# Kernel tuning notes

Hardware: AMD Instinct MI355X
Metric: run time of the kernel (lower is better)

## Reference

```python
import jax, jax.numpy as jnp
import numpy as np

BLOCK, HALO, HEADS, DH = 8, 4, 4, 32
EPS = 1e-5


def _convT(x, w, p):
    # torch ConvTranspose2d(stride=1, padding=p) == conv with flipped/transposed kernel, padding k-1-p
    k = w.shape[-1]
    w2 = jnp.flip(w, axis=(-2, -1)).transpose(1, 0, 2, 3)  # (Cin,Cout,k,k) -> (Cout,Cin,k,k)
    pad = k - 1 - p
    return jax.lax.conv_general_dilated(x, w2, (1, 1), ((pad, pad), (pad, pad)),
                                        dimension_numbers=('NCHW', 'OIHW', 'NCHW'))


def _bn(x, g, b, m, v):
    s = g * jax.lax.rsqrt(v + EPS)
    return x * s[None, :, None, None] + (b - m * s)[None, :, None, None]


def _rel_to_abs(x):
    # x: [b, l, 2r-1] -> [b, l, r]
    b, l, m = x.shape
    r = (m + 1) // 2
    x = jnp.concatenate([x, jnp.zeros((b, l, 1), x.dtype)], axis=2)
    flat = jnp.concatenate([x.reshape(b, l * (m + 1)), jnp.zeros((b, m - l), x.dtype)], axis=1)
    return flat.reshape(b, l + 1, m)[:, :l, -r:]


def _rel_logits_1d(q, rel_k):
    # q: [b, x, y, d]; rel_k: [2r-1, d] -> [b, x, r, y, r]
    b, x, y, d = q.shape
    r = (rel_k.shape[0] + 1) // 2
    logits = jnp.einsum('bxyd,rd->bxyr', q, rel_k)
    logits = _rel_to_abs(logits.reshape(b * x, y, -1)).reshape(b, x, y, r)
    return jnp.broadcast_to(logits[:, :, None, :, :], (b, x, r, y, r))


def _rel_pos_emb(q, rel_h, rel_w):
    # q: [bb, block*block, dh] (already scaled, per halonet-pytorch)
    bb, n, d = q.shape
    qg = q.reshape(bb, BLOCK, BLOCK, d)
    lw = _rel_logits_1d(qg, rel_w).transpose(0, 1, 3, 2, 4).reshape(bb, n, -1)  # b (x y) (i j)
    lh = _rel_logits_1d(qg.transpose(0, 2, 1, 3), rel_h).transpose(0, 3, 1, 4, 2).reshape(bb, n, -1)  # b (y x) (j i)
    return lw + lh


def _halo_attn(x, to_q, to_kv, to_out_w, to_out_b, rel_h, rel_w):
    B, C, H, W = x.shape
    b, h = BLOCK, HALO
    nh, nw = H // b, W // b
    nblk = nh * nw
    wsz = b + 2 * h
    inner = to_q.shape[1]
    scale = DH ** -0.5
    # queries: non-overlapping blocks -> [B*nblk, b*b, C]
    q_inp = x.reshape(B, C, nh, b, nw, b).transpose(0, 2, 4, 3, 5, 1).reshape(B * nblk, b * b, C)
    # keys/values: overlapping halo windows (F.unfold) -> [B*nblk, wsz*wsz, C]
    pat = jax.lax.conv_general_dilated_patches(x, (wsz, wsz), (b, b), ((h, h), (h, h)))  # [B, C*wsz*wsz, nh, nw]
    kv_inp = pat.reshape(B, C, wsz * wsz, nblk).transpose(0, 3, 2, 1).reshape(B * nblk, wsz * wsz, C)
    q = q_inp @ to_q
    k, v = jnp.split(kv_inp @ to_kv, 2, axis=-1)
    def heads(t):
        return t.reshape(t.shape[0], t.shape[1], HEADS, DH).transpose(0, 2, 1, 3).reshape(-1, t.shape[1], DH)
    q, k, v = heads(q) * scale, heads(k), heads(v)
    sim = jnp.einsum('bid,bjd->bij', q, k) + _rel_pos_emb(q, rel_h, rel_w)  # [B*nblk*HEADS, b*b, wsz*wsz]
    # mask out halo positions that fall into zero padding
    ones = jnp.ones((1, 1, H, W), x.dtype)
    mpat = jax.lax.conv_general_dilated_patches(ones, (wsz, wsz), (b, b), ((h, h), (h, h)))
    mask = mpat.reshape(wsz * wsz, nblk).T > 0  # [nblk, wsz*wsz]
    neg = -jnp.finfo(sim.dtype).max
    sim = jnp.where(mask[None, :, None, None, :],
                    sim.reshape(B, nblk, HEADS, b * b, wsz * wsz), neg)
    attn = jax.nn.softmax(sim, axis=-1).reshape(-1, b * b, wsz * wsz)
    out = jnp.einsum('bij,bjd->bid', attn, v)
    out = out.reshape(B * nblk, HEADS, b * b, DH).transpose(0, 2, 1, 3).reshape(B * nblk, b * b, inner)
    out = out @ to_out_w + to_out_b
    return out.reshape(B, nh, nw, b, b, C).transpose(0, 5, 1, 3, 2, 4).reshape(B, C, H, W)


def setup_inputs() -> dict:
    key = jax.random.key(0)
    ks = jax.random.split(key, 13)
    B, C, H, W = 2, 128, 192, 192
    inner = HEADS * DH
    rel = 2 * (BLOCK + 2 * HALO) - 1  # 31
    n = lambda k, s, sc: jax.random.normal(k, s, jnp.float32) * sc
    return {
        'x': jax.random.normal(ks[0], (B, C, H, W), jnp.float32),
        'conv1_w': n(ks[1], (C, C, 1, 1), 0.1),
        'bn1_g': jnp.ones((C,), jnp.float32), 'bn1_b': jnp.zeros((C,), jnp.float32),
        'bn1_m': n(ks[2], (C,), 0.1),
        'bn1_v': jax.random.uniform(ks[3], (C,), jnp.float32, 0.5, 1.5),
        'to_q': n(ks[4], (C, inner), 0.05), 'to_kv': n(ks[5], (C, 2 * inner), 0.05),
        'to_out_w': n(ks[6], (inner, C), 0.05), 'to_out_b': n(ks[7], (C,), 0.01),
        'rel_h': n(ks[8], (rel, DH), DH ** -0.5), 'rel_w': n(ks[9], (rel, DH), DH ** -0.5),
        'conv3_w': n(ks[10], (C, C, 3, 3), 0.05),
        'bn3_g': jnp.ones((C,), jnp.float32), 'bn3_b': jnp.zeros((C,), jnp.float32),
        'bn3_m': n(ks[11], (C,), 0.1),
        'bn3_v': jax.random.uniform(ks[12], (C,), jnp.float32, 0.5, 1.5),
    }


def reference(x, conv1_w, bn1_g, bn1_b, bn1_m, bn1_v, to_q, to_kv, to_out_w, to_out_b,
              rel_h, rel_w, conv3_w, bn3_g, bn3_b, bn3_m, bn3_v):
    # Bottleneck (stride=1, no downsample): conv1x1T -> BN -> ReLU -> HaloAttention -> ReLU
    #   -> conv3x3T -> BN -> +identity -> ReLU
    out = jax.nn.relu(_bn(_convT(x, conv1_w, 0), bn1_g, bn1_b, bn1_m, bn1_v))
    out = jax.nn.relu(_halo_attn(out, to_q, to_kv, to_out_w, to_out_b, rel_h, rel_w))
    out = _bn(_convT(out, conv3_w, 1), bn3_g, bn3_b, bn3_m, bn3_v)
    return jax.nn.relu(out + x)
```

## Files before the change

### kernel.cpp

```cpp
#include <hip/hip_runtime.h>
#include <hip/hip_bf16.h>

using bf16 = __hip_bfloat16;
typedef unsigned short u16;
typedef unsigned int   u32;
typedef __attribute__((ext_vector_type(8))) short short8;
typedef __attribute__((ext_vector_type(4))) float f32x4;

#define B_N 2
#define CCH 128
#define HH 192
#define WW 192
#define HWS (HH*WW)
#define NPIX (B_N*HWS)
#define NBLKS 576
#define EPSV 1e-5f
#define LDW 136

__device__ __forceinline__ float b2f(bf16 v){ return __bfloat162float(v); }
__device__ __forceinline__ bf16  f2b(float v){ return __float2bfloat16(v); }
__device__ __forceinline__ u16  bits(bf16 v){ return *(u16*)&v; }
__device__ __forceinline__ u32 pck(float a, float b){
    bf16 x = f2b(a), y = f2b(b);
    return (u32)*(u16*)&x | ((u32)*(u16*)&y << 16);
}

__global__ __launch_bounds__(256) void transpose_in(const float* __restrict__ x,
                                                    bf16* __restrict__ xT)
{
    __shared__ float tile[128][17];
    const int t   = threadIdx.x;
    const int hw0 = blockIdx.x * 16;
    const int n   = hw0 / HWS;
    const int hwl = hw0 - n*HWS;
    const int px = t & 15, cb = t >> 4;
    #pragma unroll
    for (int r = 0; r < 8; ++r){
        int ci = r*16 + cb;
        tile[ci][px] = x[(size_t)(n*CCH + ci)*HWS + hwl + px];
    }
    __syncthreads();
    const int pix = t >> 4, cig = t & 15;
    uint4 pk;
    pk.x = pck(tile[cig*8+0][pix], tile[cig*8+1][pix]);
    pk.y = pck(tile[cig*8+2][pix], tile[cig*8+3][pix]);
    pk.z = pck(tile[cig*8+4][pix], tile[cig*8+5][pix]);
    pk.w = pck(tile[cig*8+6][pix], tile[cig*8+7][pix]);
    *(uint4*)&xT[(size_t)(hw0 + pix)*CCH + cig*8] = pk;
}

__global__ __launch_bounds__(256) void prep_w(
    const float* __restrict__ w1, const float* __restrict__ to_q,
    const float* __restrict__ to_kv, const float* __restrict__ to_ow,
    const float* __restrict__ w3, const float* __restrict__ relh,
    const float* __restrict__ relw, bf16* __restrict__ wb)
{
    int i = blockIdx.x*256 + threadIdx.x;
    if (i >= 231360) return;
    float v;
    if (i < 16384){       int co=(i>>7)&127, ci=i&127;      v = w1[ci*128+co]; }
    else if (i < 32768){  int r=i-16384; int co=r>>7, ci=r&127; v = to_q[ci*128+co]*0.17677669529663687f; }
    else if (i < 49152){  int r=i-32768; int co=r>>7, ci=r&127; v = to_kv[ci*256+co]; }
    else if (i < 65536){  int r=i-49152; int co=r>>7, ci=r&127; v = to_kv[ci*256+128+co]; }
    else if (i < 81920){  int r=i-65536; int co=r>>7, ci=r&127; v = to_ow[ci*128+co]; }
    else if (i < 229376){ int r=i-81920; int tap=r>>14, co=(r>>7)&127, ci=r&127; int a=tap/3, b=tap-a*3;
                          v = w3[((size_t)(ci*128+co)*3+a)*3+b]; }
    else if (i < 230368){ v = relh[i-229376]; }
    else                { v = relw[i-230368]; }
    wb[i] = f2b(v);
}

template<bool DO_BN, bool DO_BIAS, bool DO_RELU, bool TRANS_Y2>
__global__ __launch_bounds__(256) void gemm_mfma(
    const bf16* __restrict__ inp, const bf16* __restrict__ Wp,
    bf16* __restrict__ outp, bf16* __restrict__ outp2, int cstride, int choff,
    const float* __restrict__ bn_g, const float* __restrict__ bn_b,
    const float* __restrict__ bn_m, const float* __restrict__ bn_v,
    const float* __restrict__ bias)
{
    Wp    += (size_t)blockIdx.y * 16384;
    choff += blockIdx.y * 128;
    __shared__ u16 sW[128*LDW];
    __shared__ u16 sX[64*LDW];
    const int tid  = threadIdx.x;
    const int pix0 = blockIdx.x * 64;
    const int lane = tid & 63;
    const int ln = lane & 15, g = lane >> 4;
    const int cow = (tid >> 6) * 32;

    #pragma unroll
    for (int r = 0; r < 8; ++r){
        int e = tid + r*256; int row = e>>4, grp = e&15;
        *(uint4*)&sW[row*LDW + grp*8] = *(const uint4*)&Wp[row*128 + grp*8];
    }
    #pragma unroll
    for (int r = 0; r < 4; ++r){
        int e = tid + r*256; int row = e>>4, grp = e&15;
        *(uint4*)&sX[row*LDW + grp*8] = *(const uint4*)&inp[(size_t)(pix0+row)*CCH + grp*8];
    }
    __syncthreads();

    f32x4 acc[4][2];
    #pragma unroll
    for (int mi=0;mi<4;mi++)
        #pragma unroll
        for (int ni=0;ni<2;ni++) acc[mi][ni] = (f32x4){0.f,0.f,0.f,0.f};

    #pragma unroll
    for (int kk = 0; kk < 4; ++kk){
        short8 fa[4], fb[2];
        #pragma unroll
        for (int mi=0;mi<4;mi++)
            fa[mi] = *(const short8*)&sX[(mi*16+ln)*LDW + kk*32 + g*8];
        #pragma unroll
        for (int ni=0;ni<2;ni++)
            fb[ni] = *(const short8*)&sW[(cow+ni*16+ln)*LDW + kk*32 + g*8];
        #pragma unroll
        for (int mi=0;mi<4;mi++)
            #pragma unroll
            for (int ni=0;ni<2;ni++)
                acc[mi][ni] = __builtin_amdgcn_mfma_f32_16x16x32_bf16(fa[mi], fb[ni], acc[mi][ni], 0, 0, 0);
    }

    if (TRANS_Y2 && blockIdx.y == 2){
        __syncthreads();
        u16* tile = sX;
        #pragma unroll
        for (int mi=0;mi<4;mi++)
            #pragma unroll
            for (int ni=0;ni<2;ni++){
                int co   = cow + ni*16 + ln;
                int pixl = mi*16 + g*4;
                *(u32*)&tile[co*68 + pixl]     = pck(acc[mi][ni][0], acc[mi][ni][1]);
                *(u32*)&tile[co*68 + pixl + 2] = pck(acc[mi][ni][2], acc[mi][ni][3]);
            }
        __syncthreads();
        const int co2 = tid >> 1, hf = tid & 1;
        const int n2 = pix0 / HWS, hwb2 = pix0 - n2*HWS;
        u16* gdst = (u16*)outp2 + (size_t)(n2*CCH + co2)*HWS + hwb2 + hf*32;
        const u16* src = &tile[co2*68 + hf*32];
        #pragma unroll
        for (int k=0;k<8;k++)
            *(uint2*)&gdst[k*4] = *(const uint2*)&src[k*4];
        return;
    }

    float sc[2], bb[2];
    #pragma unroll
    for (int ni=0;ni<2;ni++){
        int co = cow + ni*16 + ln;
        sc[ni] = 1.f; bb[ni] = 0.f;
        if (DO_BN){ float sg = bn_g[co]*rsqrtf(bn_v[co]+EPSV); sc[ni]=sg; bb[ni]=bn_b[co]-bn_m[co]*sg; }
        if (DO_BIAS) bb[ni] += bias[co];
    }
    #pragma unroll
    for (int mi=0;mi<4;mi++)
        #pragma unroll
        for (int ni=0;ni<2;ni++)
            #pragma unroll
            for (int j=0;j<4;j++){
                int pix = pix0 + mi*16 + g*4 + j;
                int co  = cow + ni*16 + ln;
                float v = acc[mi][ni][j]*sc[ni] + bb[ni];
                if (DO_RELU) v = fmaxf(v, 0.f);
                outp[(size_t)pix*cstride + choff + co] = f2b(v);
            }
}

__global__ __launch_bounds__(256) void conv3_mfma(
    const bf16* __restrict__ inp, const bf16* __restrict__ W3p,
    const float* __restrict__ xin, float* __restrict__ outp,
    const float* __restrict__ g3, const float* __restrict__ b3,
    const float* __restrict__ m3, const float* __restrict__ v3)
{
    __shared__ u16 sW[128*LDW];
    __shared__ u16 sX[64*LDW];
    const int tid = threadIdx.x;
    const int P0  = blockIdx.x * 64;
    const int n   = P0 / HWS;
    const int hwb = P0 - n*HWS;
    const int h = hwb / WW, wb = hwb - h*WW;
    const int lane = tid & 63, ln = lane & 15, g = lane >> 4;
    const int cow = (tid >> 6) * 32;

    f32x4 acc[2][4];
    #pragma unroll
    for (int mi=0;mi<2;mi++)
        #pragma unroll
        for (int ni=0;ni<4;ni++) acc[mi][ni] = (f32x4){0.f,0.f,0.f,0.f};

    for (int tap = 0; tap < 9; ++tap){
        const int a = tap/3, b = tap - a*3;
        const int hs = h + 1 - a;
        if (hs < 0 || hs >= HH) continue;
        const int ws0 = wb + 1 - b;
        __syncthreads();
        #pragma unroll
        for (int r = 0; r < 8; ++r){
            int e = tid + r*256; int row = e>>4, grp = e&15;
            *(uint4*)&sW[row*LDW + grp*8] = *(const uint4*)&W3p[tap*16384 + row*128 + grp*8];
        }
        #pragma unroll
        for (int r = 0; r < 4; ++r){
            int e = tid + r*256; int row = e>>4, grp = e&15;
            int wsrc = ws0 + row;
            uint4 val = {0u,0u,0u,0u};
            if (wsrc >= 0 && wsrc < WW)
                val = *(const uint4*)&inp[(size_t)(n*HWS + hs*WW + wsrc)*CCH + grp*8];
            *(uint4*)&sX[row*LDW + grp*8] = val;
        }
        __syncthreads();
        #pragma unroll
        for (int kk = 0; kk < 4; ++kk){
            short8 fa[2], fb[4];
            #pragma unroll
            for (int mi=0;mi<2;mi++)
                fa[mi] = *(const short8*)&sW[(cow+mi*16+ln)*LDW + kk*32 + g*8];
            #pragma unroll
            for (int ni=0;ni<4;ni++)
                fb[ni] = *(const short8*)&sX[(ni*16+ln)*LDW + kk*32 + g*8];
            #pragma unroll
            for (int mi=0;mi<2;mi++)
                #pragma unroll
                for (int ni=0;ni<4;ni++)
                    acc[mi][ni] = __builtin_amdgcn_mfma_f32_16x16x32_bf16(fa[mi], fb[ni], acc[mi][ni], 0, 0, 0);
        }
    }

    #pragma unroll
    for (int mi=0;mi<2;mi++)
        #pragma unroll
        for (int j=0;j<4;j++){
            int co = cow + mi*16 + g*4 + j;
            float sg = g3[co]*rsqrtf(v3[co]+EPSV);
            float bc = b3[co] - m3[co]*sg;
            #pragma unroll
            for (int ni=0;ni<4;ni++){
                int pixl = hwb + ni*16 + ln;
                size_t idx = (size_t)(n*CCH + co)*HWS + pixl;
                float v = acc[mi][ni][j]*sg + bc + xin[idx];
                outp[idx] = fmaxf(v, 0.f);
            }
        }
}

__global__ __launch_bounds__(512) void attn_kernel(
    const u16* __restrict__ QK, const u16* __restrict__ vT,
    const u16* __restrict__ relb, bf16* __restrict__ outp)
{
    __shared__ __align__(16) char smem[60160];
    u16*   sQb  = (u16*)(smem);
    u16*   sK   = (u16*)(smem + 5120);
    u16*   sRH  = (u16*)(smem + 25600);
    u16*   sRW  = (u16*)(smem + 28160);
    u16*   sP   = (u16*)(smem);
    u16*   sVT  = (u16*)(smem + 33792);
    float* tT   = (float*)(smem + 50688);
    float* wredM= (float*)(smem + 59136);
    float* wredS= (float*)(smem + 59648);

    const int tid  = threadIdx.x;
    const int bid0 = blockIdx.x;
    const int bid  = (bid0 & 7) * 576 + (bid0 >> 3);
    const int head = bid & 3;
    const int t    = bid >> 2;
    const int n    = t / NBLKS;
    const int blk  = t - n*NBLKS;
    const int bi = blk / 24, bj = blk - bi*24;
    const int row0 = bi*8 - 4, col0 = bj*8 - 4;
    const int ch0 = head*32;
    const int wv = tid >> 6, lane = tid & 63, ln = lane & 15, g = lane >> 4;
    const int nt = wv & 3, mh = wv >> 2;

    for (int e = tid; e < 1024; e += 512){
        int r = e >> 5, d = e & 31;
        sRH[r*40 + d] = (r < 31) ? relb[r*32 + d]       : (u16)0;
        sRW[r*40 + d] = (r < 31) ? relb[992 + r*32 + d] : (u16)0;
    }
    {
        int qq = tid >> 3, db = tid & 7;
        size_t P = (size_t)n*HWS + (bi*8 + (qq>>3))*WW + bj*8 + (qq&7);
        *(uint2*)&sQb[qq*40 + db*4] = *(const uint2*)&QK[P*256 + ch0 + db*4];
    }
    #pragma unroll
    for (int r = 0; r < 4; ++r){
        int e = tid + r*512;
        int wp = e >> 3, db = e & 7;
        int rr = row0 + (wp>>4), cc2 = col0 + (wp&15);
        uint2 kk2 = {0u,0u};
        if (rr>=0 && rr<HH && cc2>=0 && cc2<WW){
            size_t P = (size_t)n*HWS + rr*WW + cc2;
            kk2 = *(const uint2*)&QK[P*256 + 128 + ch0 + db*4];
        }
        *(uint2*)&sK[wp*40 + db*4] = kk2;
    }
    #pragma unroll
    for (int r = 0; r < 4; ++r){
        int e = tid + r*512;
        int d   = e >> 6;
        int rem = e & 63;
        int iw  = rem >> 2;
        int jc  = (rem & 3) * 4;
        int rr  = row0 + iw, cc0 = col0 + jc;
        uint2 vv = {0u,0u};
        if (rr >= 0 && rr < HH && cc0 >= 0 && cc0 < 189)
            vv = *(const uint2*)&vT[(size_t)(n*CCH + ch0 + d)*HWS + rr*WW + cc0];
        *(uint2*)&sVT[d*264 + iw*16 + jc] = vv;
    }
    __syncthreads();

    const short8 qfrag = *(const short8*)&sQb[(nt*16+ln)*40 + g*8];
    f32x4 accs[8];
    #pragma unroll
    for (int i=0;i<8;i++){
        short8 fk = *(const short8*)&sK[((mh*8+i)*16+ln)*40 + g*8];
        accs[i] = __builtin_amdgcn_mfma_f32_16x16x32_bf16(fk, qfrag, (f32x4){0.f,0.f,0.f,0.f}, 0, 0, 0);
    }

    {
        const u16* sRX = mh ? sRW : sRH;
        #pragma unroll
        for (int ntr=0; ntr<2; ++ntr){
            short8 fr = *(const short8*)&sRX[(ntr*16+ln)*40 + g*8];
            f32x4 L = __builtin_amdgcn_mfma_f32_16x16x32_bf16(qfrag, fr, (f32x4){0.f,0.f,0.f,0.f}, 0, 0, 0);
            #pragma unroll
            for (int r2=0;r2<4;r2++){
                int q  = nt*16 + g*4 + r2;
                int rr = ntr*16 + ln;
                int bq = mh ? (q&7) : (q>>3);
                int iw = rr - 15 + bq;
                if (iw >= 0 && iw < 16) tT[mh*1056 + iw*66 + q] = L[r2];
            }
        }
    }
    __syncthreads();

    const int qc = nt*16 + ln;
    float tw[4];
    bool cok[4];
    #pragma unroll
    for (int r2=0;r2<4;r2++){
        tw[r2] = tT[1056 + (g*4+r2)*66 + qc];
        int cc2 = col0 + g*4 + r2;
        cok[r2] = (cc2 >= 0 && cc2 < WW);
    }
    float mx = -3.4e38f;
    #pragma unroll
    for (int i=0;i<8;i++){
        int mt = mh*8 + i;
        int rr = row0 + mt;
        bool rok = (rr >= 0 && rr < HH);
        float th = tT[mt*66 + qc];
        #pragma unroll
        for (int r2=0;r2<4;r2++){
            float s = (rok && cok[r2]) ? (accs[i][r2] + th + tw[r2]) : -3.0e38f;
            accs[i][r2] = s;
            mx = fmaxf(mx, s);
        }
    }
    mx = fmaxf(mx, __shfl_xor(mx, 16));
    mx = fmaxf(mx, __shfl_xor(mx, 32));
    if (g == 0) wredM[mh*64 + qc] = mx;
    __syncthreads();
    mx = fmaxf(wredM[qc], wredM[64 + qc]);

    float sm = 0.f;
    #pragma unroll
    for (int i=0;i<8;i++){
        int mt = mh*8 + i;
        float p0 = __expf(accs[i][0]-mx);
        float p1 = __expf(accs[i][1]-mx);
        float p2 = __expf(accs[i][2]-mx);
        float p3 = __expf(accs[i][3]-mx);
        sm += (p0+p1)+(p2+p3);
        u32* dst = (u32*)&sP[qc*264 + mt*16 + g*4];
        dst[0] = pck(p0,p1);
        dst[1] = pck(p2,p3);
    }
    sm += __shfl_xor(sm, 16);
    sm += __shfl_xor(sm, 32);
    if (g == 0) wredS[mh*64 + qc] = sm;
    __syncthreads();

    const int dt = wv & 1, qt = wv >> 1;
    f32x4 acco = (f32x4){0.f,0.f,0.f,0.f};
    #pragma unroll
    for (int ks=0; ks<8; ++ks){
        short8 fa = *(const short8*)&sVT[(dt*16+ln)*264 + ks*32 + g*8];
        short8 fb = *(const short8*)&sP [(qt*16+ln)*264 + ks*32 + g*8];
        acco = __builtin_amdgcn_mfma_f32_16x16x32_bf16(fa, fb, acco, 0, 0, 0);
    }
    {
        const int q = qt*16 + ln;
        const float inv = 1.f / (wredS[q] + wredS[64 + q]);
        size_t P = (size_t)n*HWS + (bi*8 + (q>>3))*WW + bj*8 + (q&7);
        uint2 ov;
        ov.x = pck(acco[0]*inv, acco[1]*inv);
        ov.y = pck(acco[2]*inv, acco[3]*inv);
        *(uint2*)&outp[P*CCH + ch0 + dt*16 + g*4] = ov;
    }
}

extern "C" void kernel_launch(void* const* d_in, const int* in_sizes, int n_in,
                              void* d_out, int out_size, void* d_ws, size_t ws_size,
                              hipStream_t stream)
{
    (void)in_sizes; (void)n_in; (void)out_size; (void)ws_size;
    const float* x      = (const float*)d_in[0];
    const float* w1     = (const float*)d_in[1];
    const float* bn1_g  = (const float*)d_in[2];
    const float* bn1_b  = (const float*)d_in[3];
    const float* bn1_m  = (const float*)d_in[4];
    const float* bn1_v  = (const float*)d_in[5];
    const float* to_q   = (const float*)d_in[6];
    const float* to_kv  = (const float*)d_in[7];
    const float* to_ow  = (const float*)d_in[8];
    const float* to_ob  = (const float*)d_in[9];
    const float* rel_h  = (const float*)d_in[10];
    const float* rel_w  = (const float*)d_in[11];
    const float* w3     = (const float*)d_in[12];
    const float* bn3_g  = (const float*)d_in[13];
    const float* bn3_b  = (const float*)d_in[14];
    const float* bn3_m  = (const float*)d_in[15];
    const float* bn3_v  = (const float*)d_in[16];

    char* ws   = (char*)d_ws;
    bf16* out1 = (bf16*)(ws + 0);
    bf16* qk   = (bf16*)(ws + 18874368);
    bf16* xT   = (bf16*)(ws + 56623104);
    bf16* vT   = (bf16*)(ws + 75497472);
    bf16* wb   = (bf16*)(ws + 94371840);
    bf16* W3p  = wb + 81920;
    u16*  relb = (u16*)(wb + 229376);
    bf16* attnout = (bf16*)d_out;
    bf16* out2    = out1;

    transpose_in<<<4608, 256, 0, stream>>>(x, xT);
    prep_w<<<904, 256, 0, stream>>>(w1, to_q, to_kv, to_ow, w3, rel_h, rel_w, wb);

    gemm_mfma<true,false,true,false><<<dim3(1152,1), 256, 0, stream>>>(
        xT, wb, out1, nullptr, 128, 0, bn1_g, bn1_b, bn1_m, bn1_v, nullptr);
    gemm_mfma<false,false,false,true><<<dim3(1152,3), 256, 0, stream>>>(
        out1, wb + 16384, qk, vT, 256, 0, nullptr,nullptr,nullptr,nullptr,nullptr);

    attn_kernel<<<4608, 512, 0, stream>>>((const u16*)qk, (const u16*)vT,
                                          relb, attnout);

    gemm_mfma<false,true,true,false><<<dim3(1152,1), 256, 0, stream>>>(
        attnout, wb + 65536, out2, nullptr, 128, 0, nullptr,nullptr,nullptr,nullptr, to_ob);

    conv3_mfma<<<1152, 256, 0, stream>>>(out2, W3p, x, (float*)d_out,
                                         bn3_g, bn3_b, bn3_m, bn3_v);
}
```

Measured before the change: 185.3 us.

## Fuse input transpose into conv1 GEMM and shrink attention shared memory

Removes the separate transpose_in kernel: conv1_mfma now reads the fp32 NCHW input directly, transposes and converts it to bf16 in shared memory, and runs the 1x1 conv GEMM with BN+ReLU in the same kernel. The aim is to cut one launch and the round trip of the xT intermediate through global memory. The attention kernel loads Q and the relative-position tables straight from global memory instead of staging them in LDS, and pads the rel tables in prep_w to 32 rows. It also splits the P·V product into two halves that reuse a half-size sP buffer, which adds syncs but reduces LDS use to raise occupancy.

```diff
diff --git a/kernel.cpp b/kernel.cpp
--- a/kernel.cpp
+++ b/kernel.cpp
@@ -12,41 +12,15 @@
 #define HH 192
 #define WW 192
 #define HWS (HH*WW)
-#define NPIX (B_N*HWS)
 #define NBLKS 576
 #define EPSV 1e-5f
 #define LDW 136
 
 __device__ __forceinline__ float b2f(bf16 v){ return __bfloat162float(v); }
 __device__ __forceinline__ bf16  f2b(float v){ return __float2bfloat16(v); }
-__device__ __forceinline__ u16  bits(bf16 v){ return *(u16*)&v; }
 __device__ __forceinline__ u32 pck(float a, float b){
     bf16 x = f2b(a), y = f2b(b);
     return (u32)*(u16*)&x | ((u32)*(u16*)&y << 16);
-}
-
-__global__ __launch_bounds__(256) void transpose_in(const float* __restrict__ x,
-                                                    bf16* __restrict__ xT)
-{
-    __shared__ float tile[128][17];
-    const int t   = threadIdx.x;
-    const int hw0 = blockIdx.x * 16;
-    const int n   = hw0 / HWS;
-    const int hwl = hw0 - n*HWS;
-    const int px = t & 15, cb = t >> 4;
-    #pragma unroll
-    for (int r = 0; r < 8; ++r){
-        int ci = r*16 + cb;
-        tile[ci][px] = x[(size_t)(n*CCH + ci)*HWS + hwl + px];
-    }
-    __syncthreads();
-    const int pix = t >> 4, cig = t & 15;
-    uint4 pk;
-    pk.x = pck(tile[cig*8+0][pix], tile[cig*8+1][pix]);
-    pk.y = pck(tile[cig*8+2][pix], tile[cig*8+3][pix]);
-    pk.z = pck(tile[cig*8+4][pix], tile[cig*8+5][pix]);
-    pk.w = pck(tile[cig*8+6][pix], tile[cig*8+7][pix]);
-    *(uint4*)&xT[(size_t)(hw0 + pix)*CCH + cig*8] = pk;
 }
 
 __global__ __launch_bounds__(256) void prep_w(
@@ -56,7 +30,6 @@
     const float* __restrict__ relw, bf16* __restrict__ wb)
 {
     int i = blockIdx.x*256 + threadIdx.x;
-    if (i >= 231360) return;
     float v;
     if (i < 16384){       int co=(i>>7)&127, ci=i&127;      v = w1[ci*128+co]; }
     else if (i < 32768){  int r=i-16384; int co=r>>7, ci=r&127; v = to_q[ci*128+co]*0.17677669529663687f; }
@@ -65,17 +38,99 @@
     else if (i < 81920){  int r=i-65536; int co=r>>7, ci=r&127; v = to_ow[ci*128+co]; }
     else if (i < 229376){ int r=i-81920; int tap=r>>14, co=(r>>7)&127, ci=r&127; int a=tap/3, b=tap-a*3;
                           v = w3[((size_t)(ci*128+co)*3+a)*3+b]; }
-    else if (i < 230368){ v = relh[i-229376]; }
-    else                { v = relw[i-230368]; }
+    else if (i < 230400){ int j=i-229376; v = (j < 992) ? relh[j] : 0.f; }
+    else                { int j=i-230400; v = (j < 992) ? relw[j] : 0.f; }
     wb[i] = f2b(v);
 }
 
-template<bool DO_BN, bool DO_BIAS, bool DO_RELU, bool TRANS_Y2>
+__global__ __launch_bounds__(256) void conv1_mfma(
+    const float* __restrict__ x, const bf16* __restrict__ Wp,
+    bf16* __restrict__ outp,
+    const float* __restrict__ bn_g, const float* __restrict__ bn_b,
+    const float* __restrict__ bn_m, const float* __restrict__ bn_v)
+{
+    __shared__ float tF[128*68];
+    __shared__ u16   sX[64*LDW];
+    u16* sW = (u16*)tF;
+    const int tid  = threadIdx.x;
+    const int pix0 = blockIdx.x * 64;
+    const int n    = pix0 / HWS;
+    const int hwb  = pix0 - n*HWS;
+    const int lane = tid & 63;
+    const int ln = lane & 15, g = lane >> 4;
+    const int cow = (tid >> 6) * 32;
+
+    #pragma unroll
+    for (int r = 0; r < 32; ++r){
+        int e = tid + r*256;
+        int ci = e >> 6, px = e & 63;
+        tF[ci*68 + px] = x[(size_t)(n*CCH + ci)*HWS + hwb + px];
+    }
+    __syncthreads();
+    {
+        const int pix = tid & 63, cq = tid >> 6;
+        u32 pkt[16];
+        #pragma unroll
+        for (int c = 0; c < 16; ++c){
+            int ci = cq*32 + c*2;
+            pkt[c] = pck(tF[ci*68 + pix], tF[(ci+1)*68 + pix]);
+        }
+        u32* dst = (u32*)&sX[pix*LDW + cq*32];
+        #pragma unroll
+        for (int c = 0; c < 16; ++c) dst[c] = pkt[c];
+    }
+    __syncthreads();
+    #pragma unroll
+    for (int r = 0; r < 8; ++r){
+        int e = tid + r*256; int row = e>>4, grp = e&15;
+        *(uint4*)&sW[row*LDW + grp*8] = *(const uint4*)&Wp[row*128 + grp*8];
+    }
+    __syncthreads();
+
+    f32x4 acc[4][2];
+    #pragma unroll
+    for (int mi=0;mi<4;mi++)
+        #pragma unroll
+        for (int ni=0;ni<2;ni++) acc[mi][ni] = (f32x4){0.f,0.f,0.f,0.f};
+    #pragma unroll
+    for (int kk = 0; kk < 4; ++kk){
+        short8 fa[4], fb[2];
+        #pragma unroll
+        for (int mi=0;mi<4;mi++)
+            fa[mi] = *(const short8*)&sX[(mi*16+ln)*LDW + kk*32 + g*8];
+        #pragma unroll
+        for (int ni=0;ni<2;ni++)
+            fb[ni] = *(const short8*)&sW[(cow+ni*16+ln)*LDW + kk*32 + g*8];
+        #pragma unroll
+        for (int mi=0;mi<4;mi++)
+            #pragma unroll
+            for (int ni=0;ni<2;ni++)
+                acc[mi][ni] = __builtin_amdgcn_mfma_f32_16x16x32_bf16(fa[mi], fb[ni], acc[mi][ni], 0, 0, 0);
+    }
+    float sc[2], bb[2];
+    #pragma unroll
+    for (int ni=0;ni<2;ni++){
+        int co = cow + ni*16 + ln;
+        float sg = bn_g[co]*rsqrtf(bn_v[co]+EPSV);
+        sc[ni] = sg; bb[ni] = bn_b[co] - bn_m[co]*sg;
+    }
+    #pragma unroll
+    for (int mi=0;mi<4;mi++)
+        #pragma unroll
+        for (int ni=0;ni<2;ni++)
+            #pragma unroll
+            for (int j=0;j<4;j++){
+                int pix = pix0 + mi*16 + g*4 + j;
+                int co  = cow + ni*16 + ln;
+                float v = fmaxf(acc[mi][ni][j]*sc[ni] + bb[ni], 0.f);
+                outp[(size_t)pix*CCH + co] = f2b(v);
+            }
+}
+
+template<bool DO_BIAS, bool DO_RELU, bool TRANS_Y2>
 __global__ __launch_bounds__(256) void gemm_mfma(
     const bf16* __restrict__ inp, const bf16* __restrict__ Wp,
     bf16* __restrict__ outp, bf16* __restrict__ outp2, int cstride, int choff,
-    const float* __restrict__ bn_g, const float* __restrict__ bn_b,
-    const float* __restrict__ bn_m, const float* __restrict__ bn_v,
     const float* __restrict__ bias)
 {
     Wp    += (size_t)blockIdx.y * 16384;
@@ -145,13 +200,11 @@
         return;
     }
 
-    float sc[2], bb[2];
+    float bb[2];
     #pragma unroll
     for (int ni=0;ni<2;ni++){
         int co = cow + ni*16 + ln;
-        sc[ni] = 1.f; bb[ni] = 0.f;
-        if (DO_BN){ float sg = bn_g[co]*rsqrtf(bn_v[co]+EPSV); sc[ni]=sg; bb[ni]=bn_b[co]-bn_m[co]*sg; }
-        if (DO_BIAS) bb[ni] += bias[co];
+        bb[ni] = DO_BIAS ? bias[co] : 0.f;
     }
     #pragma unroll
     for (int mi=0;mi<4;mi++)
@@ -161,7 +214,7 @@
             for (int j=0;j<4;j++){
                 int pix = pix0 + mi*16 + g*4 + j;
                 int co  = cow + ni*16 + ln;
-                float v = acc[mi][ni][j]*sc[ni] + bb[ni];
+                float v = acc[mi][ni][j] + bb[ni];
                 if (DO_RELU) v = fmaxf(v, 0.f);
                 outp[(size_t)pix*cstride + choff + co] = f2b(v);
             }
@@ -248,16 +301,13 @@
     const u16* __restrict__ QK, const u16* __restrict__ vT,
     const u16* __restrict__ relb, bf16* __restrict__ outp)
 {
-    __shared__ __align__(16) char smem[60160];
-    u16*   sQb  = (u16*)(smem);
-    u16*   sK   = (u16*)(smem + 5120);
-    u16*   sRH  = (u16*)(smem + 25600);
-    u16*   sRW  = (u16*)(smem + 28160);
+    __shared__ __align__(16) char smem[46848];
+    u16*   sK   = (u16*)(smem);
     u16*   sP   = (u16*)(smem);
-    u16*   sVT  = (u16*)(smem + 33792);
-    float* tT   = (float*)(smem + 50688);
-    float* wredM= (float*)(smem + 59136);
-    float* wredS= (float*)(smem + 59648);
+    u16*   sVT  = (u16*)(smem + 20480);
+    float* tT   = (float*)(smem + 37376);
+    float* wredM= (float*)(smem + 45824);
+    float* wredS= (float*)(smem + 46336);
 
     const int tid  = threadIdx.x;
     const int bid0 = blockIdx.x;
@@ -272,16 +322,6 @@
     const int wv = tid >> 6, lane = tid & 63, ln = lane & 15, g = lane >> 4;
     const int nt = wv & 3, mh = wv >> 2;
 
-    for (int e = tid; e < 1024; e += 512){
-        int r = e >> 5, d = e & 31;
-        sRH[r*40 + d] = (r < 31) ? relb[r*32 + d]       : (u16)0;
-        sRW[r*40 + d] = (r < 31) ? relb[992 + r*32 + d] : (u16)0;
-    }
-    {
-        int qq = tid >> 3, db = tid & 7;
-        size_t P = (size_t)n*HWS + (bi*8 + (qq>>3))*WW + bj*8 + (qq&7);
-        *(uint2*)&sQb[qq*40 + db*4] = *(const uint2*)&QK[P*256 + ch0 + db*4];
-    }
     #pragma unroll
     for (int r = 0; r < 4; ++r){
         int e = tid + r*512;
@@ -307,9 +347,12 @@
             vv = *(const uint2*)&vT[(size_t)(n*CCH + ch0 + d)*HWS + rr*WW + cc0];
         *(uint2*)&sVT[d*264 + iw*16 + jc] = vv;
     }
-    __syncthreads();
-
-    const short8 qfrag = *(const short8*)&sQb[(nt*16+ln)*40 + g*8];
+
+    const int qc = nt*16 + ln;
+    size_t Pq = (size_t)n*HWS + (bi*8 + (qc>>3))*WW + bj*8 + (qc&7);
+    const short8 qfrag = *(const short8*)&QK[Pq*256 + ch0 + g*8];
+    __syncthreads();
+
     f32x4 accs[8];
     #pragma unroll
     for (int i=0;i<8;i++){
@@ -318,10 +361,10 @@
     }
 
     {
-        const u16* sRX = mh ? sRW : sRH;
+        const u16* relX = relb + (mh ? 1024 : 0);
         #pragma unroll
         for (int ntr=0; ntr<2; ++ntr){
-            short8 fr = *(const short8*)&sRX[(ntr*16+ln)*40 + g*8];
+            short8 fr = *(const short8*)&relX[(ntr*16+ln)*32 + g*8];
             f32x4 L = __builtin_amdgcn_mfma_f32_16x16x32_bf16(qfrag, fr, (f32x4){0.f,0.f,0.f,0.f}, 0, 0, 0);
             #pragma unroll
             for (int r2=0;r2<4;r2++){
@@ -335,7 +378,6 @@
     }
     __syncthreads();
 
-    const int qc = nt*16 + ln;
     float tw[4];
     bool cok[4];
     #pragma unroll
@@ -367,27 +409,49 @@
     float sm = 0.f;
     #pragma unroll
     for (int i=0;i<8;i++){
-        int mt = mh*8 + i;
-        float p0 = __expf(accs[i][0]-mx);
-        float p1 = __expf(accs[i][1]-mx);
-        float p2 = __expf(accs[i][2]-mx);
-        float p3 = __expf(accs[i][3]-mx);
-        sm += (p0+p1)+(p2+p3);
-        u32* dst = (u32*)&sP[qc*264 + mt*16 + g*4];
-        dst[0] = pck(p0,p1);
-        dst[1] = pck(p2,p3);
+        #pragma unroll
+        for (int r2=0;r2<4;r2++){
+            float p = __expf(accs[i][r2] - mx);
+            accs[i][r2] = p;
+            sm += p;
+        }
     }
     sm += __shfl_xor(sm, 16);
     sm += __shfl_xor(sm, 32);
     if (g == 0) wredS[mh*64 + qc] = sm;
+    if (mh == 0){
+        #pragma unroll
+        for (int i=0;i<8;i++){
+            u32* dst = (u32*)&sP[qc*136 + i*16 + g*4];
+            dst[0] = pck(accs[i][0], accs[i][1]);
+            dst[1] = pck(accs[i][2], accs[i][3]);
+        }
+    }
     __syncthreads();
 
     const int dt = wv & 1, qt = wv >> 1;
     f32x4 acco = (f32x4){0.f,0.f,0.f,0.f};
     #pragma unroll
-    for (int ks=0; ks<8; ++ks){
+    for (int ks=0; ks<4; ++ks){
         short8 fa = *(const short8*)&sVT[(dt*16+ln)*264 + ks*32 + g*8];
-        short8 fb = *(const short8*)&sP [(qt*16+ln)*264 + ks*32 + g*8];
+        short8 fb = *(const short8*)&sP [(qt*16+ln)*136 + ks*32 + g*8];
+        acco = __builtin_amdgcn_mfma_f32_16x16x32_bf16(fa, fb, acco, 0, 0, 0);
+    }
+    __syncthreads();
+    if (mh == 1){
+        #pragma unroll
+        for (int i=0;i<8;i++){
+            u32* dst = (u32*)&sP[qc*136 + i*16 + g*4];
+            dst[0] = pck(accs[i][0], accs[i][1]);
+            dst[1] = pck(accs[i][2], accs[i][3]);
+        }
+    }
+    __syncthreads();
+
+    #pragma unroll
+    for (int ks=0; ks<4; ++ks){
+        short8 fa = *(const short8*)&sVT[(dt*16+ln)*264 + 128 + ks*32 + g*8];
+        short8 fb = *(const short8*)&sP [(qt*16+ln)*136 + ks*32 + g*8];
         acco = __builtin_amdgcn_mfma_f32_16x16x32_bf16(fa, fb, acco, 0, 0, 0);
     }
     {
@@ -427,7 +491,6 @@
     char* ws   = (char*)d_ws;
     bf16* out1 = (bf16*)(ws + 0);
     bf16* qk   = (bf16*)(ws + 18874368);
-    bf16* xT   = (bf16*)(ws + 56623104);
     bf16* vT   = (bf16*)(ws + 75497472);
     bf16* wb   = (bf16*)(ws + 94371840);
     bf16* W3p  = wb + 81920;
@@ -435,19 +498,17 @@
     bf16* attnout = (bf16*)d_out;
     bf16* out2    = out1;
 
-    transpose_in<<<4608, 256, 0, stream>>>(x, xT);
     prep_w<<<904, 256, 0, stream>>>(w1, to_q, to_kv, to_ow, w3, rel_h, rel_w, wb);
 
-    gemm_mfma<true,false,true,false><<<dim3(1152,1), 256, 0, stream>>>(
-        xT, wb, out1, nullptr, 128, 0, bn1_g, bn1_b, bn1_m, bn1_v, nullptr);
-    gemm_mfma<false,false,false,true><<<dim3(1152,3), 256, 0, stream>>>(
-        out1, wb + 16384, qk, vT, 256, 0, nullptr,nullptr,nullptr,nullptr,nullptr);
+    conv1_mfma<<<1152, 256, 0, stream>>>(x, wb, out1, bn1_g, bn1_b, bn1_m, bn1_v);
+    gemm_mfma<false,false,true><<<dim3(1152,3), 256, 0, stream>>>(
+        out1, wb + 16384, qk, vT, 256, 0, nullptr);
 
     attn_kernel<<<4608, 512, 0, stream>>>((const u16*)qk, (const u16*)vT,
                                           relb, attnout);
 
-    gemm_mfma<false,true,true,false><<<dim3(1152,1), 256, 0, stream>>>(
-        attnout, wb + 65536, out2, nullptr, 128, 0, nullptr,nullptr,nullptr,nullptr, to_ob);
+    gemm_mfma<true,true,false><<<dim3(1152,1), 256, 0, stream>>>(
+        attnout, wb + 65536, out2, nullptr, 128, 0, to_ob);
 
     conv3_mfma<<<1152, 256, 0, stream>>>(out2, W3p, x, (float*)d_out,
                                          bn3_g, bn3_b, bn3_m, bn3_v);
```

Result: faster. 164.7 us (-11.1%).
